# Performance work log

Measured on AMD Instinct MI355X. Metric: run time of the kernel, lower is better.

The kernel has to match this reference:

```python
import jax, jax.numpy as jnp
import numpy as np

N_NODES = 100000
N_EDGES = 3200000
N_CLASSES = 16
P = 2  # p-norm order


def setup_inputs() -> dict:
    key = jax.random.key(0)
    k1, k2, k3 = jax.random.split(key, 3)
    edge_index = jax.random.randint(k1, (2, N_EDGES), 0, N_NODES, dtype=jnp.int64)
    edge_weights = jax.random.uniform(k2, (N_EDGES,), dtype=jnp.float32)
    y = jax.random.normal(k3, (N_NODES, N_CLASSES), dtype=jnp.float32)
    return {"edge_index": edge_index, "edge_weights": edge_weights, "y": y}


def reference(edge_index, edge_weights, y):
    row, col = edge_index[0], edge_index[1]
    n = y.shape[0]
    # sym normalization: degree = row-sum of weighted adjacency (O(E) segment sum,
    # replacing the original dense NxN materialization)
    degree = jax.ops.segment_sum(edge_weights, row, num_segments=n)
    d = jnp.sqrt(degree)
    d_r = d[row][:, None]  # (E,1)
    d_c = d[col][:, None]
    diff = y[row] / d_r - y[col] / d_c  # (E,C)
    pnorm = jnp.sum(jnp.abs(diff) ** P, axis=1) ** (1.0 / P)  # (E,)
    return jnp.mean(pnorm * edge_weights)
```

## Files before the change

### kernel.cpp

```cpp
#include <hip/hip_runtime.h>

#define N_NODES   100000
#define N_CLASSES 16
#define N_EDGES   3200000

#define R_RANGES        8
#define NODES_PER_RANGE 12500
#define B_SUPER         1024
#define KE              8

#define P_SHADOW  8
#define N_PAD     100416
#define KD        10


__device__ __forceinline__ unsigned f2fp8(float f) {
    unsigned u = __float_as_uint(f);
    unsigned s = (u >> 24) & 0x80u;
    float g = fabsf(f) * 0x1p-120f;
    unsigned gu = __float_as_uint(g);
    gu += 0x7FFFFu + ((gu >> 20) & 1u);
    unsigned mag = gu >> 20;
    if (mag > 0x7Eu) mag = 0x7Eu;
    return s | mag;
}

__device__ __forceinline__ float fp82f(unsigned b) {
    unsigned u = ((b & 0x80u) << 24) | ((b & 0x7Fu) << 20);
    return __uint_as_float(u) * 0x1p120f;
}

__device__ __forceinline__ float ssd4(unsigned a, unsigned b) {
    float s = 0.0f;
#pragma unroll
    for (int i = 0; i < 4; ++i) {
        float va = fp82f((a >> (8 * i)) & 0xFFu);
        float vb = fp82f((b >> (8 * i)) & 0xFFu);
        float d = va - vb;
        s += d * d;
    }
    return s;
}


__global__ __launch_bounds__(B_SUPER) void lap_degree_super(
        const int* __restrict__ rows, const float* __restrict__ w,
        float* __restrict__ shadows, int eps ) {
    __shared__ float hist[NODES_PER_RANGE];
    const int r  = blockIdx.x & (R_RANGES - 1);
    const int s  = blockIdx.x >> 3;
    const int lo = r * NODES_PER_RANGE;

    for (int i = threadIdx.x; i < NODES_PER_RANGE; i += B_SUPER) hist[i] = 0.0f;
    __syncthreads();

    const int base = s * eps;
    const int ng   = eps >> 2;
    for (int g = threadIdx.x; g < ng; g += B_SUPER) {
        const int e = base + g * 4;
        int4   r4 = *(const int4*)(rows + e);
        float4 w4 = *(const float4*)(w + e);
        int t;
        t = r4.x - lo; if ((unsigned)t < (unsigned)NODES_PER_RANGE) atomicAdd(&hist[t], w4.x);
        t = r4.y - lo; if ((unsigned)t < (unsigned)NODES_PER_RANGE) atomicAdd(&hist[t], w4.y);
        t = r4.z - lo; if ((unsigned)t < (unsigned)NODES_PER_RANGE) atomicAdd(&hist[t], w4.z);
        t = r4.w - lo; if ((unsigned)t < (unsigned)NODES_PER_RANGE) atomicAdd(&hist[t], w4.w);
    }
    __syncthreads();

    float* dst = shadows + (size_t)s * N_NODES + lo;
    for (int i = threadIdx.x; i < NODES_PER_RANGE; i += B_SUPER) dst[i] = hist[i];
}


__global__ void lap_yhat_super(const float* __restrict__ shadows,
                               const float* __restrict__ y,
                               unsigned char* __restrict__ yhat, int S) {
    const int n = blockIdx.x * blockDim.x + threadIdx.x;
    if (n >= N_NODES) return;
    float deg = 0.0f;
    for (int s = 0; s < S; ++s) deg += shadows[(size_t)s * N_NODES + n];
    const float inv = rsqrtf(deg);

    const float4* yr = (const float4*)(y + (size_t)n * N_CLASSES);
    uint4 o;
    unsigned* op = (unsigned*)&o;
#pragma unroll
    for (int j = 0; j < 4; ++j) {
        float4 v = yr[j];
        op[j] =  f2fp8(v.x * inv)
              | (f2fp8(v.y * inv) << 8)
              | (f2fp8(v.z * inv) << 16)
              | (f2fp8(v.w * inv) << 24);
    }
    *(uint4*)(yhat + (size_t)n * N_CLASSES) = o;
}


__global__ void lap_degree_p(const int* __restrict__ rows,
                             const float* __restrict__ w,
                             float* __restrict__ degp) {
    const int tid = blockIdx.x * blockDim.x + threadIdx.x;
    float* mydeg = degp + (size_t)(blockIdx.x & (P_SHADOW - 1)) * N_PAD;
    int   r[KD];
    float wv[KD];
#pragma unroll
    for (int k = 0; k < KD; ++k) {
        int e = tid + k * (N_EDGES / KD);
        r[k]  = rows[e];
        wv[k] = w[e];
    }
#pragma unroll
    for (int k = 0; k < KD; ++k) atomicAdd(&mydeg[r[k]], wv[k]);
}

__global__ void lap_yhat_mid(const float* __restrict__ degp,
                             const float* __restrict__ y,
                             unsigned char* __restrict__ yhat) {
    const int n = blockIdx.x * blockDim.x + threadIdx.x;
    if (n >= N_NODES) return;
    float deg = 0.0f;
#pragma unroll
    for (int p = 0; p < P_SHADOW; ++p) deg += degp[(size_t)p * N_PAD + n];
    const float inv = rsqrtf(deg);
    const float4* yr = (const float4*)(y + (size_t)n * N_CLASSES);
    uint4 o;
    unsigned* op = (unsigned*)&o;
#pragma unroll
    for (int j = 0; j < 4; ++j) {
        float4 v = yr[j];
        op[j] =  f2fp8(v.x * inv)
              | (f2fp8(v.y * inv) << 8)
              | (f2fp8(v.z * inv) << 16)
              | (f2fp8(v.w * inv) << 24);
    }
    *(uint4*)(yhat + (size_t)n * N_CLASSES) = o;
}


__global__ void lap_edge_fp8(const int* __restrict__ rows,
                             const int* __restrict__ cols,
                             const float* __restrict__ w,
                             const unsigned char* __restrict__ yhat,
                             float* __restrict__ acc) {
    const int tid = blockIdx.x * blockDim.x + threadIdx.x;
    const long e0 = (long)tid * KE;
    float local = 0.0f;
    if (e0 < N_EDGES) {
        int4   ra = *(const int4*)(rows + e0);
        int4   rb = *(const int4*)(rows + e0 + 4);
        int4   ca = *(const int4*)(cols + e0);
        int4   cb = *(const int4*)(cols + e0 + 4);
        float4 wa = *(const float4*)(w + e0);
        float4 wb = *(const float4*)(w + e0 + 4);

        const int ri[KE] = {ra.x, ra.y, ra.z, ra.w, rb.x, rb.y, rb.z, rb.w};
        const int ci[KE] = {ca.x, ca.y, ca.z, ca.w, cb.x, cb.y, cb.z, cb.w};
        const float wv[KE] = {wa.x, wa.y, wa.z, wa.w, wb.x, wb.y, wb.z, wb.w};

        uint4 A[KE], B[KE];
#pragma unroll
        for (int k = 0; k < KE; ++k) {
            A[k] = *(const uint4*)(yhat + (size_t)ri[k] * N_CLASSES);
            B[k] = *(const uint4*)(yhat + (size_t)ci[k] * N_CLASSES);
        }
#pragma unroll
        for (int k = 0; k < KE; ++k) {
            float s = ssd4(A[k].x, B[k].x) + ssd4(A[k].y, B[k].y)
                    + ssd4(A[k].z, B[k].z) + ssd4(A[k].w, B[k].w);
            local += wv[k] * sqrtf(s);
        }
    }
#pragma unroll
    for (int off = 32; off > 0; off >>= 1) local += __shfl_down(local, off, 64);
    __shared__ float sm[4];
    const int lane = threadIdx.x & 63;
    const int wid  = threadIdx.x >> 6;
    if (lane == 0) sm[wid] = local;
    __syncthreads();
    if (threadIdx.x == 0) atomicAdd(acc, sm[0] + sm[1] + sm[2] + sm[3]);
}

__global__ void lap_final_kernel(const float* __restrict__ acc,
                                 float* __restrict__ out) {
    out[0] = acc[0] * (1.0f / (float)N_EDGES);
}


__global__ void lap_degree_kernel(const int* __restrict__ rows,
                                  const float* __restrict__ w,
                                  float* __restrict__ degree) {
    int i = blockIdx.x * blockDim.x + threadIdx.x;
    if (i < N_EDGES) atomicAdd(&degree[rows[i]], w[i]);
}

__global__ void lap_invd_kernel(const float* __restrict__ degree,
                                float* __restrict__ invd) {
    int i = blockIdx.x * blockDim.x + threadIdx.x;
    if (i < N_NODES) invd[i] = rsqrtf(degree[i]);
}

__global__ void lap_edge_kernel(const int* __restrict__ rows,
                                const int* __restrict__ cols,
                                const float* __restrict__ w,
                                const float* __restrict__ y,
                                const float* __restrict__ invd,
                                float* __restrict__ acc) {
    int i = blockIdx.x * blockDim.x + threadIdx.x;
    float local = 0.0f;
    if (i < N_EDGES) {
        int r = rows[i], c = cols[i];
        float dr = invd[r], dc = invd[c];
        const float4* yr = (const float4*)(y + (size_t)r * N_CLASSES);
        const float4* yc = (const float4*)(y + (size_t)c * N_CLASSES);
        float s = 0.0f;
#pragma unroll
        for (int j = 0; j < N_CLASSES / 4; ++j) {
            float4 a = yr[j], b = yc[j];
            float d0 = a.x * dr - b.x * dc;
            float d1 = a.y * dr - b.y * dc;
            float d2 = a.z * dr - b.z * dc;
            float d3 = a.w * dr - b.w * dc;
            s += d0 * d0 + d1 * d1 + d2 * d2 + d3 * d3;
        }
        local = w[i] * sqrtf(s);
    }
#pragma unroll
    for (int off = 32; off > 0; off >>= 1) local += __shfl_down(local, off, 64);
    __shared__ float sm[4];
    int lane = threadIdx.x & 63, wid = threadIdx.x >> 6;
    if (lane == 0) sm[wid] = local;
    __syncthreads();
    if (threadIdx.x == 0) atomicAdd(acc, sm[0] + sm[1] + sm[2] + sm[3]);
}


extern "C" void kernel_launch(void* const* d_in, const int* in_sizes, int n_in,
                              void* d_out, int out_size, void* d_ws, size_t ws_size,
                              hipStream_t stream) {
    const int*   edge_index = (const int*)d_in[0];
    const float* w          = (const float*)d_in[1];
    const float* y          = (const float*)d_in[2];
    float*       out        = (float*)d_out;

    const int* rows = edge_index;
    const int* cols = edge_index + N_EDGES;
    const int  B = 256;

    auto need_super = [](int S) -> size_t {
        return (64 + (size_t)S * N_NODES) * sizeof(float)
             + (size_t)N_NODES * N_CLASSES;
    };
    int S = 0;
    if      (ws_size >= need_super(64)) S = 64;
    else if (ws_size >= need_super(32)) S = 32;
    else if (ws_size >= need_super(16)) S = 16;

    const size_t yhat_mid_off = (64 + (size_t)P_SHADOW * N_PAD) * sizeof(float);
    const size_t need_mid     = yhat_mid_off + (size_t)N_NODES * N_CLASSES;

    const int edge_threads = N_EDGES / KE;
    const int edge_blocks  = (edge_threads + B - 1) / B;

    if (S > 0) {
        float*         acc     = (float*)d_ws;
        float*         shadows = acc + 64;
        unsigned char* yhat    = (unsigned char*)d_ws
                               + (64 + (size_t)S * N_NODES) * sizeof(float);

        hipMemsetAsync(d_ws, 0, 256, stream);
        lap_degree_super<<<R_RANGES * S, B_SUPER, 0, stream>>>(rows, w, shadows, N_EDGES / S);
        lap_yhat_super<<<(N_NODES + B - 1) / B, B, 0, stream>>>(shadows, y, yhat, S);
        lap_edge_fp8<<<edge_blocks, B, 0, stream>>>(rows, cols, w, yhat, acc);
        lap_final_kernel<<<1, 1, 0, stream>>>(acc, out);
    } else if (ws_size >= need_mid) {
        float*         acc  = (float*)d_ws;
        float*         degp = acc + 64;
        unsigned char* yhat = (unsigned char*)d_ws + yhat_mid_off;

        hipMemsetAsync(d_ws, 0, yhat_mid_off, stream);
        lap_degree_p<<<(N_EDGES / KD) / B, B, 0, stream>>>(rows, w, degp);
        lap_yhat_mid<<<(N_NODES + B - 1) / B, B, 0, stream>>>(degp, y, yhat);
        lap_edge_fp8<<<edge_blocks, B, 0, stream>>>(rows, cols, w, yhat, acc);
        lap_final_kernel<<<1, 1, 0, stream>>>(acc, out);
    } else {
        float* degree = (float*)d_ws;
        float* acc    = degree + N_NODES;
        float* invd   = acc + 16;
        hipMemsetAsync(d_ws, 0, (size_t)(N_NODES + 16) * sizeof(float), stream);
        lap_degree_kernel<<<(N_EDGES + B - 1) / B, B, 0, stream>>>(rows, w, degree);
        lap_invd_kernel<<<(N_NODES + B - 1) / B, B, 0, stream>>>(degree, invd);
        lap_edge_kernel<<<(N_EDGES + B - 1) / B, B, 0, stream>>>(rows, cols, w, y, invd, acc);
        lap_final_kernel<<<1, 1, 0, stream>>>(acc, out);
    }
}
```

Baseline: 169.5 us.

## Use large dynamic-LDS degree histograms, fp16 shadows, and fold final scaling into edge kernel

The degree pass now uses about 130 KB of dynamic shared memory, so each block covers a third of the nodes (3 ranges × 85 edge slices) instead of 8 ranges. Each block scans fewer redundant edges, and it falls back to the static 8×64 layout if the attribute call fails. Per-slice partial degrees are written as fp16, halving shadow traffic, at the cost of precision in the partial sums. The final division kernel and the workspace accumulator memset are removed: each edge block atomically adds its scaled partial directly into a zeroed output.

```diff
diff --git a/kernel.cpp b/kernel.cpp
--- a/kernel.cpp
+++ b/kernel.cpp
@@ -1,13 +1,23 @@
 #include <hip/hip_runtime.h>
+#include <hip/hip_fp16.h>
 
 #define N_NODES   100000
 #define N_CLASSES 16
 #define N_EDGES   3200000
 
-#define R_RANGES        8
-#define NODES_PER_RANGE 12500
-#define B_SUPER         1024
-#define KE              8
+#define R_DYN     3
+#define NPR_DYN   33334
+#define DYN_BYTES (NPR_DYN * 4)
+#define S_DYN     85
+#define EPS_DYN   37648
+
+#define R_ST      8
+#define NPR_ST    12500
+#define S_ST      64
+#define EPS_ST    50000
+
+#define B_DEG     1024
+#define KE        8
 
 #define P_SHADOW  8
 #define N_PAD     100416
@@ -43,43 +53,74 @@
 }
 
 
-__global__ __launch_bounds__(B_SUPER) void lap_degree_super(
+__global__ __launch_bounds__(B_DEG) void lap_degree_dyn(
         const int* __restrict__ rows, const float* __restrict__ w,
-        float* __restrict__ shadows, int eps ) {
-    __shared__ float hist[NODES_PER_RANGE];
-    const int r  = blockIdx.x & (R_RANGES - 1);
+        __half* __restrict__ shadows) {
+    extern __shared__ float hist[];
+    const int r   = blockIdx.x % R_DYN;
+    const int s   = blockIdx.x / R_DYN;
+    const int lo  = r * NPR_DYN;
+    const int hi  = (lo + NPR_DYN < N_NODES) ? lo + NPR_DYN : N_NODES;
+    const int cnt = hi - lo;
+
+    for (int i = threadIdx.x; i < cnt; i += B_DEG) hist[i] = 0.0f;
+    __syncthreads();
+
+    const int base = s * EPS_DYN;
+    for (int g = threadIdx.x; g < EPS_DYN / 4; g += B_DEG) {
+        const int e = base + g * 4;
+        if (e >= N_EDGES) continue;
+        int4   r4 = *(const int4*)(rows + e);
+        float4 w4 = *(const float4*)(w + e);
+        int t;
+        t = r4.x - lo; if ((unsigned)t < (unsigned)cnt) atomicAdd(&hist[t], w4.x);
+        t = r4.y - lo; if ((unsigned)t < (unsigned)cnt) atomicAdd(&hist[t], w4.y);
+        t = r4.z - lo; if ((unsigned)t < (unsigned)cnt) atomicAdd(&hist[t], w4.z);
+        t = r4.w - lo; if ((unsigned)t < (unsigned)cnt) atomicAdd(&hist[t], w4.w);
+    }
+    __syncthreads();
+
+    __half* dst = shadows + (size_t)s * N_NODES + lo;
+    for (int i = threadIdx.x; i < cnt; i += B_DEG) dst[i] = __float2half(hist[i]);
+}
+
+
+__global__ __launch_bounds__(B_DEG) void lap_degree_static(
+        const int* __restrict__ rows, const float* __restrict__ w,
+        __half* __restrict__ shadows) {
+    __shared__ float hist[NPR_ST];
+    const int r  = blockIdx.x & (R_ST - 1);
     const int s  = blockIdx.x >> 3;
-    const int lo = r * NODES_PER_RANGE;
-
-    for (int i = threadIdx.x; i < NODES_PER_RANGE; i += B_SUPER) hist[i] = 0.0f;
-    __syncthreads();
-
-    const int base = s * eps;
-    const int ng   = eps >> 2;
-    for (int g = threadIdx.x; g < ng; g += B_SUPER) {
+    const int lo = r * NPR_ST;
+
+    for (int i = threadIdx.x; i < NPR_ST; i += B_DEG) hist[i] = 0.0f;
+    __syncthreads();
+
+    const int base = s * EPS_ST;
+    for (int g = threadIdx.x; g < EPS_ST / 4; g += B_DEG) {
         const int e = base + g * 4;
         int4   r4 = *(const int4*)(rows + e);
         float4 w4 = *(const float4*)(w + e);
         int t;
-        t = r4.x - lo; if ((unsigned)t < (unsigned)NODES_PER_RANGE) atomicAdd(&hist[t], w4.x);
-        t = r4.y - lo; if ((unsigned)t < (unsigned)NODES_PER_RANGE) atomicAdd(&hist[t], w4.y);
-        t = r4.z - lo; if ((unsigned)t < (unsigned)NODES_PER_RANGE) atomicAdd(&hist[t], w4.z);
-        t = r4.w - lo; if ((unsigned)t < (unsigned)NODES_PER_RANGE) atomicAdd(&hist[t], w4.w);
-    }
-    __syncthreads();
-
-    float* dst = shadows + (size_t)s * N_NODES + lo;
-    for (int i = threadIdx.x; i < NODES_PER_RANGE; i += B_SUPER) dst[i] = hist[i];
-}
-
-
-__global__ void lap_yhat_super(const float* __restrict__ shadows,
+        t = r4.x - lo; if ((unsigned)t < (unsigned)NPR_ST) atomicAdd(&hist[t], w4.x);
+        t = r4.y - lo; if ((unsigned)t < (unsigned)NPR_ST) atomicAdd(&hist[t], w4.y);
+        t = r4.z - lo; if ((unsigned)t < (unsigned)NPR_ST) atomicAdd(&hist[t], w4.z);
+        t = r4.w - lo; if ((unsigned)t < (unsigned)NPR_ST) atomicAdd(&hist[t], w4.w);
+    }
+    __syncthreads();
+
+    __half* dst = shadows + (size_t)s * N_NODES + lo;
+    for (int i = threadIdx.x; i < NPR_ST; i += B_DEG) dst[i] = __float2half(hist[i]);
+}
+
+
+__global__ void lap_yhat_super(const __half* __restrict__ shadows,
                                const float* __restrict__ y,
                                unsigned char* __restrict__ yhat, int S) {
     const int n = blockIdx.x * blockDim.x + threadIdx.x;
     if (n >= N_NODES) return;
     float deg = 0.0f;
-    for (int s = 0; s < S; ++s) deg += shadows[(size_t)s * N_NODES + n];
+    for (int s = 0; s < S; ++s) deg += __half2float(shadows[(size_t)s * N_NODES + n]);
     const float inv = rsqrtf(deg);
 
     const float4* yr = (const float4*)(y + (size_t)n * N_CLASSES);
@@ -142,7 +183,7 @@
                              const int* __restrict__ cols,
                              const float* __restrict__ w,
                              const unsigned char* __restrict__ yhat,
-                             float* __restrict__ acc) {
+                             float* __restrict__ out) {
     const int tid = blockIdx.x * blockDim.x + threadIdx.x;
     const long e0 = (long)tid * KE;
     float local = 0.0f;
@@ -178,12 +219,8 @@
     const int wid  = threadIdx.x >> 6;
     if (lane == 0) sm[wid] = local;
     __syncthreads();
-    if (threadIdx.x == 0) atomicAdd(acc, sm[0] + sm[1] + sm[2] + sm[3]);
-}
-
-__global__ void lap_final_kernel(const float* __restrict__ acc,
-                                 float* __restrict__ out) {
-    out[0] = acc[0] * (1.0f / (float)N_EDGES);
+    if (threadIdx.x == 0)
+        atomicAdd(out, (sm[0] + sm[1] + sm[2] + sm[3]) * (1.0f / (float)N_EDGES));
 }
 
 
@@ -205,7 +242,7 @@
                                 const float* __restrict__ w,
                                 const float* __restrict__ y,
                                 const float* __restrict__ invd,
-                                float* __restrict__ acc) {
+                                float* __restrict__ out) {
     int i = blockIdx.x * blockDim.x + threadIdx.x;
     float local = 0.0f;
     if (i < N_EDGES) {
@@ -231,7 +268,8 @@
     int lane = threadIdx.x & 63, wid = threadIdx.x >> 6;
     if (lane == 0) sm[wid] = local;
     __syncthreads();
-    if (threadIdx.x == 0) atomicAdd(acc, sm[0] + sm[1] + sm[2] + sm[3]);
+    if (threadIdx.x == 0)
+        atomicAdd(out, (sm[0] + sm[1] + sm[2] + sm[3]) * (1.0f / (float)N_EDGES));
 }
 
 
@@ -247,50 +285,46 @@
     const int* cols = edge_index + N_EDGES;
     const int  B = 256;
 
-    auto need_super = [](int S) -> size_t {
-        return (64 + (size_t)S * N_NODES) * sizeof(float)
-             + (size_t)N_NODES * N_CLASSES;
-    };
-    int S = 0;
-    if      (ws_size >= need_super(64)) S = 64;
-    else if (ws_size >= need_super(32)) S = 32;
-    else if (ws_size >= need_super(16)) S = 16;
-
-    const size_t yhat_mid_off = (64 + (size_t)P_SHADOW * N_PAD) * sizeof(float);
+    const size_t sh_bytes   = (size_t)S_DYN * N_NODES * sizeof(__half);
+    const size_t need_super = sh_bytes + (size_t)N_NODES * N_CLASSES;
+
+    const size_t yhat_mid_off = (size_t)P_SHADOW * N_PAD * sizeof(float);
     const size_t need_mid     = yhat_mid_off + (size_t)N_NODES * N_CLASSES;
 
-    const int edge_threads = N_EDGES / KE;
-    const int edge_blocks  = (edge_threads + B - 1) / B;
-
-    if (S > 0) {
-        float*         acc     = (float*)d_ws;
-        float*         shadows = acc + 64;
-        unsigned char* yhat    = (unsigned char*)d_ws
-                               + (64 + (size_t)S * N_NODES) * sizeof(float);
-
-        hipMemsetAsync(d_ws, 0, 256, stream);
-        lap_degree_super<<<R_RANGES * S, B_SUPER, 0, stream>>>(rows, w, shadows, N_EDGES / S);
-        lap_yhat_super<<<(N_NODES + B - 1) / B, B, 0, stream>>>(shadows, y, yhat, S);
-        lap_edge_fp8<<<edge_blocks, B, 0, stream>>>(rows, cols, w, yhat, acc);
-        lap_final_kernel<<<1, 1, 0, stream>>>(acc, out);
+    const int edge_blocks = (N_EDGES / KE + B - 1) / B;
+
+    hipMemsetAsync(d_out, 0, sizeof(float), stream);
+
+    if (ws_size >= need_super) {
+        __half*        shadows = (__half*)d_ws;
+        unsigned char* yhat    = (unsigned char*)d_ws + sh_bytes;
+
+        hipError_t attr_ok = hipFuncSetAttribute(
+            reinterpret_cast<const void*>(lap_degree_dyn),
+            hipFuncAttributeMaxDynamicSharedMemorySize, DYN_BYTES);
+
+        if (attr_ok == hipSuccess) {
+            lap_degree_dyn<<<R_DYN * S_DYN, B_DEG, DYN_BYTES, stream>>>(rows, w, shadows);
+            lap_yhat_super<<<(N_NODES + B - 1) / B, B, 0, stream>>>(shadows, y, yhat, S_DYN);
+        } else {
+            lap_degree_static<<<R_ST * S_ST, B_DEG, 0, stream>>>(rows, w, shadows);
+            lap_yhat_super<<<(N_NODES + B - 1) / B, B, 0, stream>>>(shadows, y, yhat, S_ST);
+        }
+        lap_edge_fp8<<<edge_blocks, B, 0, stream>>>(rows, cols, w, yhat, out);
     } else if (ws_size >= need_mid) {
-        float*         acc  = (float*)d_ws;
-        float*         degp = acc + 64;
+        float*         degp = (float*)d_ws;
         unsigned char* yhat = (unsigned char*)d_ws + yhat_mid_off;
 
         hipMemsetAsync(d_ws, 0, yhat_mid_off, stream);
         lap_degree_p<<<(N_EDGES / KD) / B, B, 0, stream>>>(rows, w, degp);
         lap_yhat_mid<<<(N_NODES + B - 1) / B, B, 0, stream>>>(degp, y, yhat);
-        lap_edge_fp8<<<edge_blocks, B, 0, stream>>>(rows, cols, w, yhat, acc);
-        lap_final_kernel<<<1, 1, 0, stream>>>(acc, out);
+        lap_edge_fp8<<<edge_blocks, B, 0, stream>>>(rows, cols, w, yhat, out);
     } else {
         float* degree = (float*)d_ws;
-        float* acc    = degree + N_NODES;
-        float* invd   = acc + 16;
-        hipMemsetAsync(d_ws, 0, (size_t)(N_NODES + 16) * sizeof(float), stream);
+        float* invd   = degree + N_NODES;
+        hipMemsetAsync(d_ws, 0, (size_t)N_NODES * sizeof(float), stream);
         lap_degree_kernel<<<(N_EDGES + B - 1) / B, B, 0, stream>>>(rows, w, degree);
         lap_invd_kernel<<<(N_NODES + B - 1) / B, B, 0, stream>>>(degree, invd);
-        lap_edge_kernel<<<(N_EDGES + B - 1) / B, B, 0, stream>>>(rows, cols, w, y, invd, acc);
-        lap_final_kernel<<<1, 1, 0, stream>>>(acc, out);
-    }
-}
+        lap_edge_kernel<<<(N_EDGES + B - 1) / B, B, 0, stream>>>(rows, cols, w, y, invd, out);
+    }
+}
```

After: 164.0 us. 1.03x faster.
